# Kernel optimization log

Hardware: AMD Instinct MI355X
Metric: run time of the kernel (lower is better)

Reference implementation:

```python
import jax, jax.numpy as jnp
import numpy as np


def _trilinear_sample(src, iz, iy, ix):
    """grid_sample 3D, mode='bilinear' (trilinear), padding_mode='zeros', on unnormalized voxel coords.
    src: [B,C,D,H,W]; iz,iy,ix: [B,D,H,W] float voxel coords (iz indexes D, iy H, ix W)."""
    B, C, D, H, W = src.shape
    z0 = jnp.floor(iz); y0 = jnp.floor(iy); x0 = jnp.floor(ix)
    tz = iz - z0; ty = iy - y0; tx = ix - x0
    z0i = z0.astype(jnp.int32); y0i = y0.astype(jnp.int32); x0i = x0.astype(jnp.int32)
    src_flat = src.reshape(B, C, D * H * W)

    def corner(dz, dy, dx):
        zc = z0i + dz; yc = y0i + dy; xc = x0i + dx
        valid = (zc >= 0) & (zc < D) & (yc >= 0) & (yc < H) & (xc >= 0) & (xc < W)
        zcc = jnp.clip(zc, 0, D - 1); ycc = jnp.clip(yc, 0, H - 1); xcc = jnp.clip(xc, 0, W - 1)
        lin = (zcc * H + ycc) * W + xcc                      # [B,D,H,W] flat spatial index
        vals = jax.vmap(lambda v, i: v[:, i.ravel()])(src_flat, lin)  # [B,C,D*H*W]
        vals = vals.reshape(B, C, D, H, W)
        wz = tz if dz else (1.0 - tz)
        wy = ty if dy else (1.0 - ty)
        wx = tx if dx else (1.0 - tx)
        w = (wz * wy * wx) * valid.astype(src.dtype)         # zeros padding
        return vals * w[:, None]

    out = jnp.zeros_like(src)
    for dz in (0, 1):
        for dy in (0, 1):
            for dx in (0, 1):
                out = out + corner(dz, dy, dx)
    return out


def reference(src, flow):
    B, _, D, H, W = flow.shape
    dt = flow.dtype
    # identity grid, channels ordered (z,y,x) i.e. (D,H,W), matching torch.meshgrid indexing='ij'
    gz, gy, gx = jnp.meshgrid(jnp.arange(D, dtype=dt), jnp.arange(H, dtype=dt),
                              jnp.arange(W, dtype=dt), indexing='ij')
    grid = jnp.stack([gz, gy, gx])[None]                     # [1,3,D,H,W]
    coords = grid + flow                                      # absolute voxel coords
    denom = jnp.array([D - 1, H - 1, W - 1], dtype=dt).reshape(1, 3, 1, 1, 1)
    norm = 2.0 * (coords / denom - 0.5)                       # normalized to [-1,1]
    # grid_sample expects last-dim order (x,y,z); align_corners=True unnormalization:
    ix = (norm[:, 2] + 1.0) * (W - 1) * 0.5
    iy = (norm[:, 1] + 1.0) * (H - 1) * 0.5
    iz = (norm[:, 0] + 1.0) * (D - 1) * 0.5
    return _trilinear_sample(src, iz, iy, ix)


def setup_inputs() -> dict:
    key = jax.random.key(0)
    k1, k2 = jax.random.split(key)
    B, C, D, H, W = 2, 2, 128, 160, 128
    src = jax.random.normal(k1, (B, C, D, H, W), dtype=jnp.float32)
    flow = jax.random.normal(k2, (B, 3, D, H, W), dtype=jnp.float32)
    return {"src": src, "flow": flow}
```

## Files before the change

kernel.cpp:

```cpp
#include <hip/hip_runtime.h>


#define B_ 2
#define C_ 2
#define D_ 128
#define H_ 160
#define W_ 128
constexpr int S_ = D_ * H_ * W_;

#define ZT 4
#define YT 4
#define XT 32
#define RZ 3
#define RY 3
#define RX 4
#define CZ (ZT + 2 * RZ)
#define CY (YT + 2 * RY)
#define CX (XT + 2 * RX)
#define NTHREADS 512
#define NCHUNK (CZ * CY * (CX / 2))

__device__ __forceinline__ float pair_val(const float* p, bool hi0, bool lo1,
                                          float wx0, float wx1) {
    const float v0 = hi0 ? p[1] : p[0];
    const float v1 = lo1 ? p[0] : p[1];
    return wx0 * v0 + wx1 * v1;
}

__device__ __forceinline__ float2 lds_pair2(const float* t, int o,
                                            bool hi0, bool lo1,
                                            float wx0, float wx1) {
    const float2 a = *(const float2*)&t[o];
    const float2 b = *(const float2*)&t[o + 2];
    const float v00 = hi0 ? b.x : a.x;
    const float v01 = lo1 ? a.x : b.x;
    const float v10 = hi0 ? b.y : a.y;
    const float v11 = lo1 ? a.y : b.y;
    return make_float2(wx0 * v00 + wx1 * v01, wx0 * v10 + wx1 * v11);
}

__global__ __launch_bounds__(NTHREADS, 8) void warp3d_tile(
    const float* __restrict__ src,
    const float* __restrict__ flow,
    float* __restrict__ out)
{
    __shared__ float tile[CZ * CY * CX * 2];

    const int tid = threadIdx.x;
    const int xb = blockIdx.x * XT;
    const int yb = blockIdx.y * YT;
    const int bz = blockIdx.z;
    const int zb = (bz & 31) * ZT;
    const int b  = bz >> 5;

    const float* fb = flow + (long long)b * 3 * S_;
    const float* s0 = src + (long long)b * C_ * S_;
    float* o0       = out + (long long)b * C_ * S_;

    const int lx = tid & 31, ly = (tid >> 5) & 3, lz = tid >> 7;
    const int x = xb + lx, y = yb + ly, z = zb + lz;
    const int s = ((z * H_ + y) << 7) + x;
    const float fz = fb[s], fy = fb[S_ + s], fx = fb[2 * S_ + s];

#pragma unroll
    for (int j = 0; j < 4; ++j) {
        const int lin = j * NTHREADS + tid;
        if (lin < NCHUNK) {
            const int row = lin / 20;
            const int c   = lin - row * 20;
            const int rz = row / CY, ry = row - rz * CY;
            const int gz = zb - RZ + rz;
            const int gy = yb - RY + ry;
            const int gx = xb - RX + c * 2;
            if ((unsigned)gz < (unsigned)D_ && (unsigned)gy < (unsigned)H_ &&
                (unsigned)gx <= (unsigned)(W_ - 2)) {
                const int off = ((gz * H_ + gy) << 7) + gx;
                const float2 va = *(const float2*)(s0 + off);
                const float2 vb = *(const float2*)(s0 + S_ + off);
                *(float4*)&tile[lin * 4] = make_float4(va.x, vb.x, va.y, vb.y);
            }
        }
    }
    __syncthreads();

    const int zlo = max(0, zb - RZ), zhi = min(D_, zb + ZT + RZ);
    const int ylo = max(0, yb - RY), yhi = min(H_, yb + YT + RY);
    const int xlo = max(0, xb - RX), xhi = min(W_, xb + XT + RX);

    const float iz = (float)z + fz;
    const float iy = (float)y + fy;
    const float ix = (float)x + fx;

    const float zf = floorf(iz), yf = floorf(iy), xf = floorf(ix);
    const float tz = iz - zf, ty = iy - yf, tx = ix - xf;
    const int z0 = (int)zf, y0 = (int)yf, x0 = (int)xf;

    const int zc0 = min(max(z0, 0), D_ - 1), zc1 = min(max(z0 + 1, 0), D_ - 1);
    const int yc0 = min(max(y0, 0), H_ - 1), yc1 = min(max(y0 + 1, 0), H_ - 1);
    const int xp  = min(max(x0, 0), W_ - 2);

    const float wz0 = ((unsigned)z0       < (unsigned)D_) ? (1.f - tz) : 0.f;
    const float wz1 = ((unsigned)(z0 + 1) < (unsigned)D_) ? tz         : 0.f;
    const float wy0 = ((unsigned)y0       < (unsigned)H_) ? (1.f - ty) : 0.f;
    const float wy1 = ((unsigned)(y0 + 1) < (unsigned)H_) ? ty         : 0.f;
    const float wx0 = ((unsigned)x0       < (unsigned)W_) ? (1.f - tx) : 0.f;
    const float wx1 = ((unsigned)(x0 + 1) < (unsigned)W_) ? tx         : 0.f;
    const bool hi0 = x0 > xp;
    const bool lo1 = x0 < xp;

    const bool fast = (zc0 >= zlo) & (zc1 < zhi) &
                      (yc0 >= ylo) & (yc1 < yhi) &
                      (xp >= xlo) & (xp + 1 < xhi);

    float acc0, acc1;
    if (fast) {
        const int izl0 = zc0 - (zb - RZ), izl1 = zc1 - (zb - RZ);
        const int iyl0 = yc0 - (yb - RY), iyl1 = yc1 - (yb - RY);
        const int ixl  = xp - (xb - RX);
        const int o00 = ((izl0 * CY + iyl0) * CX + ixl) * 2;
        const int o01 = ((izl0 * CY + iyl1) * CX + ixl) * 2;
        const int o10 = ((izl1 * CY + iyl0) * CX + ixl) * 2;
        const int o11 = ((izl1 * CY + iyl1) * CX + ixl) * 2;
        const float2 p00 = lds_pair2(tile, o00, hi0, lo1, wx0, wx1);
        const float2 p01 = lds_pair2(tile, o01, hi0, lo1, wx0, wx1);
        const float2 p10 = lds_pair2(tile, o10, hi0, lo1, wx0, wx1);
        const float2 p11 = lds_pair2(tile, o11, hi0, lo1, wx0, wx1);
        acc0 = wz0 * (wy0 * p00.x + wy1 * p01.x) + wz1 * (wy0 * p10.x + wy1 * p11.x);
        acc1 = wz0 * (wy0 * p00.y + wy1 * p01.y) + wz1 * (wy0 * p10.y + wy1 * p11.y);
    } else {
        const int l00 = ((zc0 * H_ + yc0) << 7) + xp;
        const int l01 = ((zc0 * H_ + yc1) << 7) + xp;
        const int l10 = ((zc1 * H_ + yc0) << 7) + xp;
        const int l11 = ((zc1 * H_ + yc1) << 7) + xp;
        const float q00 = pair_val(s0 + l00, hi0, lo1, wx0, wx1);
        const float q01 = pair_val(s0 + l01, hi0, lo1, wx0, wx1);
        const float q10 = pair_val(s0 + l10, hi0, lo1, wx0, wx1);
        const float q11 = pair_val(s0 + l11, hi0, lo1, wx0, wx1);
        const float r00 = pair_val(s0 + S_ + l00, hi0, lo1, wx0, wx1);
        const float r01 = pair_val(s0 + S_ + l01, hi0, lo1, wx0, wx1);
        const float r10 = pair_val(s0 + S_ + l10, hi0, lo1, wx0, wx1);
        const float r11 = pair_val(s0 + S_ + l11, hi0, lo1, wx0, wx1);
        acc0 = wz0 * (wy0 * q00 + wy1 * q01) + wz1 * (wy0 * q10 + wy1 * q11);
        acc1 = wz0 * (wy0 * r00 + wy1 * r01) + wz1 * (wy0 * r10 + wy1 * r11);
    }
    o0[s]      = acc0;
    o0[S_ + s] = acc1;
}

extern "C" void kernel_launch(void* const* d_in, const int* in_sizes, int n_in,
                              void* d_out, int out_size, void* d_ws, size_t ws_size,
                              hipStream_t stream) {
    const float* src  = (const float*)d_in[0];
    const float* flow = (const float*)d_in[1];
    float* out = (float*)d_out;

    dim3 grid(W_ / XT, H_ / YT, (D_ / ZT) * B_);
    warp3d_tile<<<grid, NTHREADS, 0, stream>>>(src, flow, out);
}
```

Before: 168.9 us.

## Loop each block over ten y-tiles, prefetching the next halo into registers

Each block now walks ten consecutive y-tiles instead of one, so the grid shrinks along y. While it computes the current tile from shared memory, it loads the next tile's halo and flow values into registers, then writes them to LDS between two barriers. The aim is to hide global-load latency behind compute and to spread per-block setup across more work. In exchange there are far fewer blocks in flight, two barriers per step, and higher register pressure.

```diff
diff --git a/kernel.cpp b/kernel.cpp
--- a/kernel.cpp
+++ b/kernel.cpp
@@ -19,6 +19,8 @@
 #define CX (XT + 2 * RX)
 #define NTHREADS 512
 #define NCHUNK (CZ * CY * (CX / 2))
+#define NY 10
+#define YSTEP (YT * W_)
 
 __device__ __forceinline__ float pair_val(const float* p, bool hi0, bool lo1,
                                           float wx0, float wx1) {
@@ -47,104 +49,148 @@
     __shared__ float tile[CZ * CY * CX * 2];
 
     const int tid = threadIdx.x;
-    const int xb = blockIdx.x * XT;
-    const int yb = blockIdx.y * YT;
-    const int bz = blockIdx.z;
-    const int zb = (bz & 31) * ZT;
-    const int b  = bz >> 5;
+    const int xb  = blockIdx.x * XT;
+    const int yb0 = blockIdx.y * (YT * NY);
+    const int bz  = blockIdx.z;
+    const int zb  = (bz & 31) * ZT;
+    const int b   = bz >> 5;
 
     const float* fb = flow + (long long)b * 3 * S_;
     const float* s0 = src + (long long)b * C_ * S_;
     float* o0       = out + (long long)b * C_ * S_;
 
-    const int lx = tid & 31, ly = (tid >> 5) & 3, lz = tid >> 7;
-    const int x = xb + lx, y = yb + ly, z = zb + lz;
-    const int s = ((z * H_ + y) << 7) + x;
-    const float fz = fb[s], fy = fb[S_ + s], fx = fb[2 * S_ + s];
-
+    int offj[4];
+    int gyj[4];
+    bool vzx[4];
 #pragma unroll
     for (int j = 0; j < 4; ++j) {
         const int lin = j * NTHREADS + tid;
-        if (lin < NCHUNK) {
-            const int row = lin / 20;
-            const int c   = lin - row * 20;
-            const int rz = row / CY, ry = row - rz * CY;
-            const int gz = zb - RZ + rz;
-            const int gy = yb - RY + ry;
-            const int gx = xb - RX + c * 2;
-            if ((unsigned)gz < (unsigned)D_ && (unsigned)gy < (unsigned)H_ &&
-                (unsigned)gx <= (unsigned)(W_ - 2)) {
-                const int off = ((gz * H_ + gy) << 7) + gx;
-                const float2 va = *(const float2*)(s0 + off);
-                const float2 vb = *(const float2*)(s0 + S_ + off);
-                *(float4*)&tile[lin * 4] = make_float4(va.x, vb.x, va.y, vb.y);
-            }
-        }
+        const int row = lin / 20;
+        const int c   = lin - row * 20;
+        const int rz = row / CY, ry = row - rz * CY;
+        const int gz = zb - RZ + rz;
+        const int gx = xb - RX + c * 2;
+        gyj[j]  = yb0 - RY + ry;
+        vzx[j]  = (lin < NCHUNK) && ((unsigned)gz < (unsigned)D_) &&
+                  ((unsigned)gx <= (unsigned)(W_ - 2));
+        offj[j] = (gz * H_ + gyj[j]) * W_ + gx;
+    }
+
+    const int lx = tid & 31, ly = (tid >> 5) & 3, lz = tid >> 7;
+    const int x = xb + lx, z = zb + lz;
+    int y_c = yb0 + ly;
+    int s_c = (z * H_ + y_c) * W_ + x;
+
+    const int zlo = max(0, zb - RZ), zhi = min(D_, zb + ZT + RZ);
+    const int xlo = max(0, xb - RX), xhi = min(W_, xb + RX + XT);
+
+    float fzc = fb[s_c], fyc = fb[S_ + s_c], fxc = fb[2 * S_ + s_c];
+#pragma unroll
+    for (int j = 0; j < 4; ++j) {
+        if (vzx[j] && (unsigned)gyj[j] < (unsigned)H_) {
+            const float2 a  = *(const float2*)(s0 + offj[j]);
+            const float2 c2 = *(const float2*)(s0 + S_ + offj[j]);
+            *(float4*)&tile[tid * 4 + j * 2048] = make_float4(a.x, c2.x, a.y, c2.y);
+        }
+        offj[j] += YSTEP; gyj[j] += YT;
     }
     __syncthreads();
 
-    const int zlo = max(0, zb - RZ), zhi = min(D_, zb + ZT + RZ);
-    const int ylo = max(0, yb - RY), yhi = min(H_, yb + YT + RY);
-    const int xlo = max(0, xb - RX), xhi = min(W_, xb + XT + RX);
-
-    const float iz = (float)z + fz;
-    const float iy = (float)y + fy;
-    const float ix = (float)x + fx;
-
-    const float zf = floorf(iz), yf = floorf(iy), xf = floorf(ix);
-    const float tz = iz - zf, ty = iy - yf, tx = ix - xf;
-    const int z0 = (int)zf, y0 = (int)yf, x0 = (int)xf;
-
-    const int zc0 = min(max(z0, 0), D_ - 1), zc1 = min(max(z0 + 1, 0), D_ - 1);
-    const int yc0 = min(max(y0, 0), H_ - 1), yc1 = min(max(y0 + 1, 0), H_ - 1);
-    const int xp  = min(max(x0, 0), W_ - 2);
-
-    const float wz0 = ((unsigned)z0       < (unsigned)D_) ? (1.f - tz) : 0.f;
-    const float wz1 = ((unsigned)(z0 + 1) < (unsigned)D_) ? tz         : 0.f;
-    const float wy0 = ((unsigned)y0       < (unsigned)H_) ? (1.f - ty) : 0.f;
-    const float wy1 = ((unsigned)(y0 + 1) < (unsigned)H_) ? ty         : 0.f;
-    const float wx0 = ((unsigned)x0       < (unsigned)W_) ? (1.f - tx) : 0.f;
-    const float wx1 = ((unsigned)(x0 + 1) < (unsigned)W_) ? tx         : 0.f;
-    const bool hi0 = x0 > xp;
-    const bool lo1 = x0 < xp;
-
-    const bool fast = (zc0 >= zlo) & (zc1 < zhi) &
-                      (yc0 >= ylo) & (yc1 < yhi) &
-                      (xp >= xlo) & (xp + 1 < xhi);
-
-    float acc0, acc1;
-    if (fast) {
-        const int izl0 = zc0 - (zb - RZ), izl1 = zc1 - (zb - RZ);
-        const int iyl0 = yc0 - (yb - RY), iyl1 = yc1 - (yb - RY);
-        const int ixl  = xp - (xb - RX);
-        const int o00 = ((izl0 * CY + iyl0) * CX + ixl) * 2;
-        const int o01 = ((izl0 * CY + iyl1) * CX + ixl) * 2;
-        const int o10 = ((izl1 * CY + iyl0) * CX + ixl) * 2;
-        const int o11 = ((izl1 * CY + iyl1) * CX + ixl) * 2;
-        const float2 p00 = lds_pair2(tile, o00, hi0, lo1, wx0, wx1);
-        const float2 p01 = lds_pair2(tile, o01, hi0, lo1, wx0, wx1);
-        const float2 p10 = lds_pair2(tile, o10, hi0, lo1, wx0, wx1);
-        const float2 p11 = lds_pair2(tile, o11, hi0, lo1, wx0, wx1);
-        acc0 = wz0 * (wy0 * p00.x + wy1 * p01.x) + wz1 * (wy0 * p10.x + wy1 * p11.x);
-        acc1 = wz0 * (wy0 * p00.y + wy1 * p01.y) + wz1 * (wy0 * p10.y + wy1 * p11.y);
-    } else {
-        const int l00 = ((zc0 * H_ + yc0) << 7) + xp;
-        const int l01 = ((zc0 * H_ + yc1) << 7) + xp;
-        const int l10 = ((zc1 * H_ + yc0) << 7) + xp;
-        const int l11 = ((zc1 * H_ + yc1) << 7) + xp;
-        const float q00 = pair_val(s0 + l00, hi0, lo1, wx0, wx1);
-        const float q01 = pair_val(s0 + l01, hi0, lo1, wx0, wx1);
-        const float q10 = pair_val(s0 + l10, hi0, lo1, wx0, wx1);
-        const float q11 = pair_val(s0 + l11, hi0, lo1, wx0, wx1);
-        const float r00 = pair_val(s0 + S_ + l00, hi0, lo1, wx0, wx1);
-        const float r01 = pair_val(s0 + S_ + l01, hi0, lo1, wx0, wx1);
-        const float r10 = pair_val(s0 + S_ + l10, hi0, lo1, wx0, wx1);
-        const float r11 = pair_val(s0 + S_ + l11, hi0, lo1, wx0, wx1);
-        acc0 = wz0 * (wy0 * q00 + wy1 * q01) + wz1 * (wy0 * q10 + wy1 * q11);
-        acc1 = wz0 * (wy0 * r00 + wy1 * r01) + wz1 * (wy0 * r10 + wy1 * r11);
+#pragma unroll 1
+    for (int t = 0; t < NY; ++t) {
+        const bool more = (t + 1 < NY);
+        float4 pn[4];
+        bool vld[4];
+        float fzn, fyn, fxn;
+
+        if (more) {
+            const int sn = s_c + YSTEP;
+            fzn = fb[sn]; fyn = fb[S_ + sn]; fxn = fb[2 * S_ + sn];
+#pragma unroll
+            for (int j = 0; j < 4; ++j) {
+                vld[j] = vzx[j] && ((unsigned)gyj[j] < (unsigned)H_);
+                if (vld[j]) {
+                    const float2 a  = *(const float2*)(s0 + offj[j]);
+                    const float2 c2 = *(const float2*)(s0 + S_ + offj[j]);
+                    pn[j] = make_float4(a.x, c2.x, a.y, c2.y);
+                }
+                offj[j] += YSTEP; gyj[j] += YT;
+            }
+        }
+
+        const int yb_c = yb0 + t * YT;
+        const int ylo = max(0, yb_c - RY), yhi = min(H_, yb_c + YT + RY);
+
+        const float iz = (float)z + fzc;
+        const float iy = (float)y_c + fyc;
+        const float ix = (float)x + fxc;
+
+        const float zf = floorf(iz), yf = floorf(iy), xf = floorf(ix);
+        const float tz = iz - zf, ty = iy - yf, tx = ix - xf;
+        const int z0 = (int)zf, y0 = (int)yf, x0 = (int)xf;
+
+        const int zc0 = min(max(z0, 0), D_ - 1), zc1 = min(max(z0 + 1, 0), D_ - 1);
+        const int yc0 = min(max(y0, 0), H_ - 1), yc1 = min(max(y0 + 1, 0), H_ - 1);
+        const int xp  = min(max(x0, 0), W_ - 2);
+
+        const float wz0 = ((unsigned)z0       < (unsigned)D_) ? (1.f - tz) : 0.f;
+        const float wz1 = ((unsigned)(z0 + 1) < (unsigned)D_) ? tz         : 0.f;
+        const float wy0 = ((unsigned)y0       < (unsigned)H_) ? (1.f - ty) : 0.f;
+        const float wy1 = ((unsigned)(y0 + 1) < (unsigned)H_) ? ty         : 0.f;
+        const float wx0 = ((unsigned)x0       < (unsigned)W_) ? (1.f - tx) : 0.f;
+        const float wx1 = ((unsigned)(x0 + 1) < (unsigned)W_) ? tx         : 0.f;
+        const bool hi0 = x0 > xp;
+        const bool lo1 = x0 < xp;
+
+        const bool fast = (zc0 >= zlo) & (zc1 < zhi) &
+                          (yc0 >= ylo) & (yc1 < yhi) &
+                          (xp >= xlo) & (xp + 1 < xhi);
+
+        float acc0, acc1;
+        if (fast) {
+            const int izl0 = zc0 - (zb - RZ), izl1 = zc1 - (zb - RZ);
+            const int iyl0 = yc0 - (yb_c - RY), iyl1 = yc1 - (yb_c - RY);
+            const int ixl  = xp - (xb - RX);
+            const int o00 = ((izl0 * CY + iyl0) * CX + ixl) * 2;
+            const int o01 = ((izl0 * CY + iyl1) * CX + ixl) * 2;
+            const int o10 = ((izl1 * CY + iyl0) * CX + ixl) * 2;
+            const int o11 = ((izl1 * CY + iyl1) * CX + ixl) * 2;
+            const float2 p00 = lds_pair2(tile, o00, hi0, lo1, wx0, wx1);
+            const float2 p01 = lds_pair2(tile, o01, hi0, lo1, wx0, wx1);
+            const float2 p10 = lds_pair2(tile, o10, hi0, lo1, wx0, wx1);
+            const float2 p11 = lds_pair2(tile, o11, hi0, lo1, wx0, wx1);
+            acc0 = wz0 * (wy0 * p00.x + wy1 * p01.x) + wz1 * (wy0 * p10.x + wy1 * p11.x);
+            acc1 = wz0 * (wy0 * p00.y + wy1 * p01.y) + wz1 * (wy0 * p10.y + wy1 * p11.y);
+        } else {
+            const int l00 = (zc0 * H_ + yc0) * W_ + xp;
+            const int l01 = (zc0 * H_ + yc1) * W_ + xp;
+            const int l10 = (zc1 * H_ + yc0) * W_ + xp;
+            const int l11 = (zc1 * H_ + yc1) * W_ + xp;
+            const float q00 = pair_val(s0 + l00, hi0, lo1, wx0, wx1);
+            const float q01 = pair_val(s0 + l01, hi0, lo1, wx0, wx1);
+            const float q10 = pair_val(s0 + l10, hi0, lo1, wx0, wx1);
+            const float q11 = pair_val(s0 + l11, hi0, lo1, wx0, wx1);
+            const float r00 = pair_val(s0 + S_ + l00, hi0, lo1, wx0, wx1);
+            const float r01 = pair_val(s0 + S_ + l01, hi0, lo1, wx0, wx1);
+            const float r10 = pair_val(s0 + S_ + l10, hi0, lo1, wx0, wx1);
+            const float r11 = pair_val(s0 + S_ + l11, hi0, lo1, wx0, wx1);
+            acc0 = wz0 * (wy0 * q00 + wy1 * q01) + wz1 * (wy0 * q10 + wy1 * q11);
+            acc1 = wz0 * (wy0 * r00 + wy1 * r01) + wz1 * (wy0 * r10 + wy1 * r11);
+        }
+        o0[s_c]      = acc0;
+        o0[S_ + s_c] = acc1;
+
+        __syncthreads();
+
+        if (more) {
+#pragma unroll
+            for (int j = 0; j < 4; ++j)
+                if (vld[j]) *(float4*)&tile[tid * 4 + j * 2048] = pn[j];
+            fzc = fzn; fyc = fyn; fxc = fxn;
+            s_c += YSTEP; y_c += YT;
+        }
+        __syncthreads();
     }
-    o0[s]      = acc0;
-    o0[S_ + s] = acc1;
 }
 
 extern "C" void kernel_launch(void* const* d_in, const int* in_sizes, int n_in,
@@ -154,6 +200,6 @@
     const float* flow = (const float*)d_in[1];
     float* out = (float*)d_out;
 
-    dim3 grid(W_ / XT, H_ / YT, (D_ / ZT) * B_);
+    dim3 grid(W_ / XT, H_ / (YT * NY), (D_ / ZT) * B_);
     warp3d_tile<<<grid, NTHREADS, 0, stream>>>(src, flow, out);
 }
```

Result: slower. 540.4 us (+219.9%).

## Replace LDS halo tiling with direct global-memory gather per voxel

Applied to the files above, without the earlier changes.

Removes the shared-memory halo tile, its cooperative load and the __syncthreads barrier. Each thread now gathers its eight corners for both channels straight from global memory, relying on L1/L2 caching for neighbour reuse. Blocks become 256 threads covering two full x-rows, with no fast/slow path split. This drops the redundant halo loads and the barrier, but gives up explicit reuse and issues more scattered global loads per voxel.

```diff
diff --git a/kernel.cpp b/kernel.cpp
--- a/kernel.cpp
+++ b/kernel.cpp
@@ -8,17 +8,7 @@
 #define W_ 128
 constexpr int S_ = D_ * H_ * W_;
 
-#define ZT 4
-#define YT 4
-#define XT 32
-#define RZ 3
-#define RY 3
-#define RX 4
-#define CZ (ZT + 2 * RZ)
-#define CY (YT + 2 * RY)
-#define CX (XT + 2 * RX)
-#define NTHREADS 512
-#define NCHUNK (CZ * CY * (CX / 2))
+#define NTHREADS 256
 
 __device__ __forceinline__ float pair_val(const float* p, bool hi0, bool lo1,
                                           float wx0, float wx1) {
@@ -27,65 +17,25 @@
     return wx0 * v0 + wx1 * v1;
 }
 
-__device__ __forceinline__ float2 lds_pair2(const float* t, int o,
-                                            bool hi0, bool lo1,
-                                            float wx0, float wx1) {
-    const float2 a = *(const float2*)&t[o];
-    const float2 b = *(const float2*)&t[o + 2];
-    const float v00 = hi0 ? b.x : a.x;
-    const float v01 = lo1 ? a.x : b.x;
-    const float v10 = hi0 ? b.y : a.y;
-    const float v11 = lo1 ? a.y : b.y;
-    return make_float2(wx0 * v00 + wx1 * v01, wx0 * v10 + wx1 * v11);
-}
-
-__global__ __launch_bounds__(NTHREADS, 8) void warp3d_tile(
+__global__ __launch_bounds__(NTHREADS, 4) void warp3d_gather(
     const float* __restrict__ src,
     const float* __restrict__ flow,
     float* __restrict__ out)
 {
-    __shared__ float tile[CZ * CY * CX * 2];
-
     const int tid = threadIdx.x;
-    const int xb = blockIdx.x * XT;
-    const int yb = blockIdx.y * YT;
+    const int x = tid & (W_ - 1);
+    const int y = blockIdx.y * 2 + (tid >> 7);
     const int bz = blockIdx.z;
-    const int zb = (bz & 31) * ZT;
-    const int b  = bz >> 5;
+    const int z = bz & (D_ - 1);
+    const int b = bz >> 7;
 
     const float* fb = flow + (long long)b * 3 * S_;
     const float* s0 = src + (long long)b * C_ * S_;
     float* o0       = out + (long long)b * C_ * S_;
 
-    const int lx = tid & 31, ly = (tid >> 5) & 3, lz = tid >> 7;
-    const int x = xb + lx, y = yb + ly, z = zb + lz;
-    const int s = ((z * H_ + y) << 7) + x;
+    const int s = (z * H_ + y) * W_ + x;
+
     const float fz = fb[s], fy = fb[S_ + s], fx = fb[2 * S_ + s];
-
-#pragma unroll
-    for (int j = 0; j < 4; ++j) {
-        const int lin = j * NTHREADS + tid;
-        if (lin < NCHUNK) {
-            const int row = lin / 20;
-            const int c   = lin - row * 20;
-            const int rz = row / CY, ry = row - rz * CY;
-            const int gz = zb - RZ + rz;
-            const int gy = yb - RY + ry;
-            const int gx = xb - RX + c * 2;
-            if ((unsigned)gz < (unsigned)D_ && (unsigned)gy < (unsigned)H_ &&
-                (unsigned)gx <= (unsigned)(W_ - 2)) {
-                const int off = ((gz * H_ + gy) << 7) + gx;
-                const float2 va = *(const float2*)(s0 + off);
-                const float2 vb = *(const float2*)(s0 + S_ + off);
-                *(float4*)&tile[lin * 4] = make_float4(va.x, vb.x, va.y, vb.y);
-            }
-        }
-    }
-    __syncthreads();
-
-    const int zlo = max(0, zb - RZ), zhi = min(D_, zb + ZT + RZ);
-    const int ylo = max(0, yb - RY), yhi = min(H_, yb + YT + RY);
-    const int xlo = max(0, xb - RX), xhi = min(W_, xb + XT + RX);
 
     const float iz = (float)z + fz;
     const float iy = (float)y + fy;
@@ -108,41 +58,23 @@
     const bool hi0 = x0 > xp;
     const bool lo1 = x0 < xp;
 
-    const bool fast = (zc0 >= zlo) & (zc1 < zhi) &
-                      (yc0 >= ylo) & (yc1 < yhi) &
-                      (xp >= xlo) & (xp + 1 < xhi);
+    const int l00 = (zc0 * H_ + yc0) * W_ + xp;
+    const int l01 = (zc0 * H_ + yc1) * W_ + xp;
+    const int l10 = (zc1 * H_ + yc0) * W_ + xp;
+    const int l11 = (zc1 * H_ + yc1) * W_ + xp;
 
-    float acc0, acc1;
-    if (fast) {
-        const int izl0 = zc0 - (zb - RZ), izl1 = zc1 - (zb - RZ);
-        const int iyl0 = yc0 - (yb - RY), iyl1 = yc1 - (yb - RY);
-        const int ixl  = xp - (xb - RX);
-        const int o00 = ((izl0 * CY + iyl0) * CX + ixl) * 2;
-        const int o01 = ((izl0 * CY + iyl1) * CX + ixl) * 2;
-        const int o10 = ((izl1 * CY + iyl0) * CX + ixl) * 2;
-        const int o11 = ((izl1 * CY + iyl1) * CX + ixl) * 2;
-        const float2 p00 = lds_pair2(tile, o00, hi0, lo1, wx0, wx1);
-        const float2 p01 = lds_pair2(tile, o01, hi0, lo1, wx0, wx1);
-        const float2 p10 = lds_pair2(tile, o10, hi0, lo1, wx0, wx1);
-        const float2 p11 = lds_pair2(tile, o11, hi0, lo1, wx0, wx1);
-        acc0 = wz0 * (wy0 * p00.x + wy1 * p01.x) + wz1 * (wy0 * p10.x + wy1 * p11.x);
-        acc1 = wz0 * (wy0 * p00.y + wy1 * p01.y) + wz1 * (wy0 * p10.y + wy1 * p11.y);
-    } else {
-        const int l00 = ((zc0 * H_ + yc0) << 7) + xp;
-        const int l01 = ((zc0 * H_ + yc1) << 7) + xp;
-        const int l10 = ((zc1 * H_ + yc0) << 7) + xp;
-        const int l11 = ((zc1 * H_ + yc1) << 7) + xp;
-        const float q00 = pair_val(s0 + l00, hi0, lo1, wx0, wx1);
-        const float q01 = pair_val(s0 + l01, hi0, lo1, wx0, wx1);
-        const float q10 = pair_val(s0 + l10, hi0, lo1, wx0, wx1);
-        const float q11 = pair_val(s0 + l11, hi0, lo1, wx0, wx1);
-        const float r00 = pair_val(s0 + S_ + l00, hi0, lo1, wx0, wx1);
-        const float r01 = pair_val(s0 + S_ + l01, hi0, lo1, wx0, wx1);
-        const float r10 = pair_val(s0 + S_ + l10, hi0, lo1, wx0, wx1);
-        const float r11 = pair_val(s0 + S_ + l11, hi0, lo1, wx0, wx1);
-        acc0 = wz0 * (wy0 * q00 + wy1 * q01) + wz1 * (wy0 * q10 + wy1 * q11);
-        acc1 = wz0 * (wy0 * r00 + wy1 * r01) + wz1 * (wy0 * r10 + wy1 * r11);
-    }
+    const float q00 = pair_val(s0 + l00, hi0, lo1, wx0, wx1);
+    const float q01 = pair_val(s0 + l01, hi0, lo1, wx0, wx1);
+    const float q10 = pair_val(s0 + l10, hi0, lo1, wx0, wx1);
+    const float q11 = pair_val(s0 + l11, hi0, lo1, wx0, wx1);
+    const float r00 = pair_val(s0 + S_ + l00, hi0, lo1, wx0, wx1);
+    const float r01 = pair_val(s0 + S_ + l01, hi0, lo1, wx0, wx1);
+    const float r10 = pair_val(s0 + S_ + l10, hi0, lo1, wx0, wx1);
+    const float r11 = pair_val(s0 + S_ + l11, hi0, lo1, wx0, wx1);
+
+    const float acc0 = wz0 * (wy0 * q00 + wy1 * q01) + wz1 * (wy0 * q10 + wy1 * q11);
+    const float acc1 = wz0 * (wy0 * r00 + wy1 * r01) + wz1 * (wy0 * r10 + wy1 * r11);
+
     o0[s]      = acc0;
     o0[S_ + s] = acc1;
 }
@@ -154,6 +86,6 @@
     const float* flow = (const float*)d_in[1];
     float* out = (float*)d_out;
 
-    dim3 grid(W_ / XT, H_ / YT, (D_ / ZT) * B_);
-    warp3d_tile<<<grid, NTHREADS, 0, stream>>>(src, flow, out);
+    dim3 grid(1, H_ / 2, D_ * B_);
+    warp3d_gather<<<grid, NTHREADS, 0, stream>>>(src, flow, out);
 }
```

Result: slower. 213.3 us (+26.3%).
